# Kernel tuning notes

Measured on AMD Instinct MI355X. Metric: run time of the kernel, lower is better.

The kernel has to match this reference:

```python
import jax, jax.numpy as jnp
import numpy as np

HIDDEN = 2048
NUM_HEADS = 16
HEAD_DIM = HIDDEN // NUM_HEADS  # 128
B, S = 2, 2048


def setup_inputs() -> dict:
    key = jax.random.key(0)
    ks = jax.random.split(key, 16)
    w = lambda k, shp: (jax.random.normal(k, shp, jnp.float32) * 0.02)
    return {
        "query": jax.random.normal(ks[0], (B, S, HIDDEN), jnp.float32),
        "key": jax.random.normal(ks[1], (B, S, HIDDEN), jnp.float32),
        "value": jax.random.normal(ks[2], (B, S, HIDDEN), jnp.float32),
        "Wq": w(ks[3], (HIDDEN, HIDDEN)), "bq": jnp.zeros((HIDDEN,), jnp.float32),
        "Wk": w(ks[4], (HIDDEN, HIDDEN)), "bk": jnp.zeros((HIDDEN,), jnp.float32),
        "Wv": w(ks[5], (HIDDEN, HIDDEN)), "bv": jnp.zeros((HIDDEN,), jnp.float32),
        "Wo": w(ks[6], (HIDDEN, HIDDEN)), "bo": jnp.zeros((HIDDEN,), jnp.float32),
        "Wf1": w(ks[7], (HEAD_DIM, 2 * HEAD_DIM)), "bf1": jnp.zeros((2 * HEAD_DIM,), jnp.float32),
        "Wf2": w(ks[8], (2 * HEAD_DIM, HEAD_DIM)), "bf2": jnp.zeros((HEAD_DIM,), jnp.float32),
    }


def reference(query, key, value, Wq, bq, Wk, bk, Wv, bv, Wo, bo, Wf1, bf1, Wf2, bf2):
    b, s, _ = query.shape

    def split_heads(x):  # [b,s,H] -> [b,h,s,d]
        return x.reshape(b, s, NUM_HEADS, HEAD_DIM).transpose(0, 2, 1, 3)

    def feature_map(x):  # MLP on last dim: d -> 2d -> relu -> d
        return jax.nn.relu(x @ Wf1 + bf1) @ Wf2 + bf2

    Q = feature_map(split_heads(query @ Wq + bq))
    K = feature_map(split_heads(key @ Wk + bk))
    V = split_heads(value @ Wv + bv)

    # K^T V per head: [b,h,d,e]
    KV = jnp.einsum("bhsd,bhse->bhde", K, V)
    QKV = jnp.einsum("bhsd,bhde->bhse", Q, KV)
    # denominator: sum of all K entries per (b,h) -> scalar per head
    denom = jnp.sum(K, axis=(-2, -1), keepdims=True) + 1e-8
    QKV = QKV / denom

    context = QKV.transpose(0, 2, 1, 3).reshape(b, s, HIDDEN)
    output = context @ Wo + bo

    attn_weights = jnp.full((b, NUM_HEADS, s, s), 1.0 / s, dtype=query.dtype)
    return output, attn_weights
```

## Files before the change

kernel.cpp:

```cpp
#include <hip/hip_runtime.h>


typedef __bf16 bf16_t;
typedef __bf16 bf16x8 __attribute__((ext_vector_type(8)));
typedef __bf16 bf16x4 __attribute__((ext_vector_type(4)));
typedef float  f32x4  __attribute__((ext_vector_type(4)));

#define FILLV (1.0f / 2048.0f)

__device__ __forceinline__ void gload16(const void* g, void* l) {
  __builtin_amdgcn_global_load_lds(
      (__attribute__((address_space(1))) void*)(g),
      (__attribute__((address_space(3))) void*)(l), 16, 0, 0);
}

template<bool RELU, bool OUTF32, bool BIAS, bool FILL>
__global__ __launch_bounds__(256) void gemm_bt(
    const bf16_t* __restrict__ A, const bf16_t* __restrict__ Bt,
    const float* __restrict__ bias, void* __restrict__ C,
    int K, int lda, int ldb, int ldc,
    long aBatchB, long aBatchH, long bBatchB, long bBatchH,
    long cBatchB, long cBatchH, int HperB,
    float* __restrict__ attn, long fillBase)
{
  __shared__ bf16_t As[128 * 64];
  __shared__ bf16_t Bs[128 * 64];

  const int z  = blockIdx.z;
  const int zb = z / HperB, zh = z % HperB;
  const bf16_t* Ab = A  + (long)zb * aBatchB + (long)zh * aBatchH
                        + (long)blockIdx.y * 128 * lda;
  const bf16_t* Bb = Bt + (long)zb * bBatchB + (long)zh * bBatchH
                        + (long)blockIdx.x * 128 * ldb;

  const int t = threadIdx.x;
  const int lane = t & 63, w = t >> 6;
  const int wm = (w >> 1) * 64, wn = (w & 1) * 64;

  f32x4 acc[4][4];
#pragma unroll
  for (int i = 0; i < 4; ++i)
#pragma unroll
    for (int j = 0; j < 4; ++j) acc[i][j] = (f32x4){0.f, 0.f, 0.f, 0.f};

  for (int k0 = 0; k0 < K; k0 += 64) {
#pragma unroll
    for (int i = 0; i < 4; ++i) {
      int c = i * 256 + t;
      int row = c >> 3, col = (c & 7) * 8;
      gload16(Ab + (long)row * lda + k0 + col, &As[c * 8]);
      gload16(Bb + (long)row * ldb + k0 + col, &Bs[c * 8]);
    }
    if constexpr (FILL) {
      const f32x4 fv = {FILLV, FILLV, FILLV, FILLV};
      const int wg = blockIdx.y * gridDim.x + blockIdx.x;
      const long nB = (long)gridDim.x * gridDim.y;
      long s0 = fillBase + (((long)(k0 >> 6) * nB + wg) * 2) * 256 + t;
      __builtin_nontemporal_store(fv, (f32x4*)attn + s0);
      __builtin_nontemporal_store(fv, (f32x4*)attn + s0 + 256);
    }
    __syncthreads();
#pragma unroll
    for (int kk = 0; kk < 2; ++kk) {
      bf16x8 af[4], bfr[4];
#pragma unroll
      for (int mi = 0; mi < 4; ++mi)
        af[mi] = *(const bf16x8*)&As[(wm + mi * 16 + (lane & 15)) * 64
                                     + kk * 32 + (lane >> 4) * 8];
#pragma unroll
      for (int ni = 0; ni < 4; ++ni)
        bfr[ni] = *(const bf16x8*)&Bs[(wn + ni * 16 + (lane & 15)) * 64
                                      + kk * 32 + (lane >> 4) * 8];
#pragma unroll
      for (int mi = 0; mi < 4; ++mi)
#pragma unroll
        for (int ni = 0; ni < 4; ++ni)
          acc[mi][ni] = __builtin_amdgcn_mfma_f32_16x16x32_bf16(
              af[mi], bfr[ni], acc[mi][ni], 0, 0, 0);
    }
    __syncthreads();
  }

  const long cb = (long)zb * cBatchB + (long)zh * cBatchH;
  const int row0 = blockIdx.y * 128 + wm;
  const int col0 = blockIdx.x * 128 + wn;
#pragma unroll
  for (int mi = 0; mi < 4; ++mi) {
#pragma unroll
    for (int ni = 0; ni < 4; ++ni) {
      const int col = col0 + ni * 16 + (lane & 15);
      const float bv = BIAS ? bias[col] : 0.f;
#pragma unroll
      for (int j = 0; j < 4; ++j) {
        const int row = row0 + mi * 16 + (lane >> 4) * 4 + j;
        float v = acc[mi][ni][j] + bv;
        if (RELU) v = fmaxf(v, 0.f);
        if (OUTF32) ((float*)C)[cb + (long)row * ldc + col] = v;
        else        ((bf16_t*)C)[cb + (long)row * ldc + col] = (bf16_t)v;
      }
    }
  }
}

__global__ __launch_bounds__(256) void proj_gemm(
    const bf16_t* __restrict__ A,
    const bf16_t* __restrict__ Wt,
    const float* __restrict__ bq, const float* __restrict__ bk,
    const float* __restrict__ bv,
    bf16_t* __restrict__ C,
    float* __restrict__ attn)
{
  __shared__ bf16_t As[128 * 64];
  __shared__ bf16_t Bs[128 * 64];

  const int t = threadIdx.x;
  const int lane = t & 63, w = t >> 6;
  const int wm = (w >> 1) * 64, wn = (w & 1) * 64;
  const int which = blockIdx.y >> 5;
  const bf16_t* Ab = A + (long)blockIdx.y * 128 * 2048;
  const bf16_t* Bb = Wt + (long)which * 4194304
                        + (long)blockIdx.x * 128 * 2048;
  const float* bias = which == 0 ? bq : (which == 1 ? bk : bv);
  const int wg = blockIdx.y * 16 + blockIdx.x;
  const f32x4 fv = {FILLV, FILLV, FILLV, FILLV};

  f32x4 acc[4][4];
#pragma unroll
  for (int i = 0; i < 4; ++i)
#pragma unroll
    for (int j = 0; j < 4; ++j) acc[i][j] = (f32x4){0.f, 0.f, 0.f, 0.f};

  for (int k0 = 0; k0 < 2048; k0 += 64) {
#pragma unroll
    for (int i = 0; i < 4; ++i) {
      int c = i * 256 + t;
      int row = c >> 3, col = (c & 7) * 8;
      gload16(Ab + (long)row * 2048 + k0 + col, &As[c * 8]);
      gload16(Bb + (long)row * 2048 + k0 + col, &Bs[c * 8]);
    }
    {
      long s0 = (((long)(k0 >> 6) * 1536 + wg) * 2) * 256 + t;
      __builtin_nontemporal_store(fv, (f32x4*)attn + s0);
      __builtin_nontemporal_store(fv, (f32x4*)attn + s0 + 256);
    }
    __syncthreads();
#pragma unroll
    for (int kk = 0; kk < 2; ++kk) {
      bf16x8 af[4], bfr[4];
#pragma unroll
      for (int mi = 0; mi < 4; ++mi)
        af[mi] = *(const bf16x8*)&As[(wm + mi * 16 + (lane & 15)) * 64
                                     + kk * 32 + (lane >> 4) * 8];
#pragma unroll
      for (int ni = 0; ni < 4; ++ni)
        bfr[ni] = *(const bf16x8*)&Bs[(wn + ni * 16 + (lane & 15)) * 64
                                      + kk * 32 + (lane >> 4) * 8];
#pragma unroll
      for (int mi = 0; mi < 4; ++mi)
#pragma unroll
        for (int ni = 0; ni < 4; ++ni)
          acc[mi][ni] = __builtin_amdgcn_mfma_f32_16x16x32_bf16(
              af[mi], bfr[ni], acc[mi][ni], 0, 0, 0);
    }
    __syncthreads();
  }

  const int row0 = blockIdx.y * 128 + wm;
  const int col0 = blockIdx.x * 128 + wn;
#pragma unroll
  for (int mi = 0; mi < 4; ++mi) {
#pragma unroll
    for (int ni = 0; ni < 4; ++ni) {
      const int col = col0 + ni * 16 + (lane & 15);
      const float bvv = bias[col];
#pragma unroll
      for (int j = 0; j < 4; ++j) {
        const int row = row0 + mi * 16 + (lane >> 4) * 4 + j;
        C[(long)row * 2048 + col] = (bf16_t)(acc[mi][ni][j] + bvv);
      }
    }
  }
}

__global__ __launch_bounds__(256) void fm_fused(
    const bf16_t* __restrict__ A, const bf16_t* __restrict__ W1t,
    const bf16_t* __restrict__ W2t, const float* __restrict__ b1,
    const float* __restrict__ b2, bf16_t* __restrict__ Out)
{
  __shared__ char Hs[64 * 256 * 2];
  const int t = threadIdx.x, lane = t & 63, w = t >> 6;
  const long r0 = (long)blockIdx.x * 64;
  const int lr = lane & 15, lk = lane >> 4;

  f32x4 acc[4][4];
#pragma unroll
  for (int i = 0; i < 4; ++i)
#pragma unroll
    for (int j = 0; j < 4; ++j) acc[i][j] = (f32x4){0.f, 0.f, 0.f, 0.f};
  const int wn = w * 64;
#pragma unroll
  for (int kk = 0; kk < 4; ++kk) {
    bf16x8 af[4], bfr[4];
#pragma unroll
    for (int mi = 0; mi < 4; ++mi)
      af[mi] = *(const bf16x8*)&A[(r0 + mi * 16 + lr) * 128 + kk * 32 + lk * 8];
#pragma unroll
    for (int ni = 0; ni < 4; ++ni)
      bfr[ni] = *(const bf16x8*)&W1t[(long)(wn + ni * 16 + lr) * 128
                                     + kk * 32 + lk * 8];
#pragma unroll
    for (int mi = 0; mi < 4; ++mi)
#pragma unroll
      for (int ni = 0; ni < 4; ++ni)
        acc[mi][ni] = __builtin_amdgcn_mfma_f32_16x16x32_bf16(
            af[mi], bfr[ni], acc[mi][ni], 0, 0, 0);
  }
#pragma unroll
  for (int ni = 0; ni < 4; ++ni) {
    const int col = wn + ni * 16 + lr;
    const float bvv = b1[col];
#pragma unroll
    for (int mi = 0; mi < 4; ++mi)
#pragma unroll
      for (int j = 0; j < 4; ++j) {
        const int row = mi * 16 + lk * 4 + j;
        float h = fmaxf(acc[mi][ni][j] + bvv, 0.f);
        int byte = (row << 9) + (col << 1);
        byte ^= (row & 7) << 4;
        *(bf16_t*)(Hs + byte) = (bf16_t)h;
      }
  }
  __syncthreads();

  f32x4 acc2[4][2];
#pragma unroll
  for (int i = 0; i < 4; ++i)
#pragma unroll
    for (int j = 0; j < 2; ++j) acc2[i][j] = (f32x4){0.f, 0.f, 0.f, 0.f};
  const int wn2 = w * 32;
#pragma unroll
  for (int kk = 0; kk < 8; ++kk) {
    bf16x8 af[4], bfr[2];
#pragma unroll
    for (int mi = 0; mi < 4; ++mi) {
      const int m = mi * 16 + lr;
      int byte = (m << 9) + kk * 64 + lk * 16;
      byte ^= (m & 7) << 4;
      af[mi] = *(const bf16x8*)(Hs + byte);
    }
#pragma unroll
    for (int ni = 0; ni < 2; ++ni)
      bfr[ni] = *(const bf16x8*)&W2t[(long)(wn2 + ni * 16 + lr) * 256
                                     + kk * 32 + lk * 8];
#pragma unroll
    for (int mi = 0; mi < 4; ++mi)
#pragma unroll
      for (int ni = 0; ni < 2; ++ni)
        acc2[mi][ni] = __builtin_amdgcn_mfma_f32_16x16x32_bf16(
            af[mi], bfr[ni], acc2[mi][ni], 0, 0, 0);
  }
#pragma unroll
  for (int ni = 0; ni < 2; ++ni) {
    const int col = wn2 + ni * 16 + lr;
    const float bvv = b2[col];
#pragma unroll
    for (int mi = 0; mi < 4; ++mi)
#pragma unroll
      for (int j = 0; j < 4; ++j) {
        const int row = mi * 16 + lk * 4 + j;
        Out[(r0 + row) * 128 + col] = (bf16_t)(acc2[mi][ni][j] + bvv);
      }
  }
}

__global__ __launch_bounds__(256) void prep(
    const float* __restrict__ q, const float* __restrict__ k,
    const float* __restrict__ v,
    const float* __restrict__ Wq, const float* __restrict__ Wk,
    const float* __restrict__ Wv, const float* __restrict__ Wo,
    const float* __restrict__ Wf1, const float* __restrict__ Wf2,
    bf16_t* __restrict__ qkv_bf, bf16_t* __restrict__ Wqkv_t,
    bf16_t* __restrict__ Wf1_t, bf16_t* __restrict__ Wf2_t)
{
  const int t = threadIdx.x;
  const int bid = blockIdx.x;
  __shared__ float tile[32][33];

  if (bid < 24576) {
    const float* in = bid < 8192 ? q : (bid < 16384 ? k : v);
    bf16_t* o = qkv_bf + (long)(bid >> 13) * 8388608L;
    long i = ((long)(bid & 8191) * 256 + t) * 4;
    float4 x = *(const float4*)&in[i];
    bf16x4 r = {(bf16_t)x.x, (bf16_t)x.y, (bf16_t)x.z, (bf16_t)x.w};
    *(bf16x4*)&o[i] = r;
    return;
  }

  const int x = t & 31, y = t >> 5;
  const float* W; bf16_t* out; int Kd, Nd, n0, k0;
  if (bid < 40960) {
    const int sub = bid - 24576;
    const int z = sub >> 12, r = sub & 4095;
    W = z == 0 ? Wq : z == 1 ? Wk : z == 2 ? Wv : Wo;
    out = Wqkv_t + (long)z * 4194304L;
    Kd = 2048; Nd = 2048;
    n0 = (r & 63) * 32; k0 = (r >> 6) * 32;
  } else if (bid < 40992) {
    const int sub = bid - 40960;
    W = Wf1; out = Wf1_t; Kd = 128; Nd = 256;
    n0 = (sub & 7) * 32; k0 = (sub >> 3) * 32;
  } else {
    const int sub = bid - 40992;
    W = Wf2; out = Wf2_t; Kd = 256; Nd = 128;
    n0 = (sub & 3) * 32; k0 = (sub >> 2) * 32;
  }
#pragma unroll
  for (int j = 0; j < 32; j += 8)
    tile[y + j][x] = W[(long)(k0 + y + j) * Nd + n0 + x];
  __syncthreads();
#pragma unroll
  for (int j = 0; j < 32; j += 8)
    out[(long)(n0 + y + j) * Kd + k0 + x] = (bf16_t)tile[x][y + j];
}

__global__ __launch_bounds__(256) void kv_partial(
    const bf16_t* __restrict__ Kf, const bf16_t* __restrict__ Vp,
    float* __restrict__ part, float* __restrict__ part_denom) {
  const int z = blockIdx.y, b = z >> 4, h = z & 15;
  const int s0 = blockIdx.x * 128;
  const int t = threadIdx.x;
  __shared__ bf16_t Ks[32 * 128];
  __shared__ bf16_t Vs[32 * 128];
  __shared__ float red[4];
  const bf16_t* Kb = Kf + (long)b * 4194304 + h * 128;
  const bf16_t* Vb = Vp + (long)b * 4194304 + h * 128;
  float acc[8][8];
#pragma unroll
  for (int i = 0; i < 8; ++i)
#pragma unroll
    for (int j = 0; j < 8; ++j) acc[i][j] = 0.f;
  float ksum = 0.f;
  const int d0 = (t & 15) * 8, e0 = (t >> 4) * 8;
  for (int sc = 0; sc < 128; sc += 32) {
#pragma unroll
    for (int i = 0; i < 2; ++i) {
      int idx = (i * 256 + t) * 8;
      int r = idx >> 7, c = idx & 127;
      long g = (long)(s0 + sc + r) * 2048 + c;
      *(bf16x8*)&Ks[r * 128 + c] = *(const bf16x8*)&Kb[g];
      *(bf16x8*)&Vs[r * 128 + c] = *(const bf16x8*)&Vb[g];
    }
    __syncthreads();
    {
      bf16x8 a0 = *(const bf16x8*)&Ks[t * 16];
      bf16x8 a1 = *(const bf16x8*)&Ks[t * 16 + 8];
#pragma unroll
      for (int j = 0; j < 8; ++j) ksum += (float)a0[j] + (float)a1[j];
    }
    for (int s = 0; s < 32; ++s) {
      bf16x8 kv = *(const bf16x8*)&Ks[s * 128 + d0];
      bf16x8 vv = *(const bf16x8*)&Vs[s * 128 + e0];
      float kf[8], vf[8];
#pragma unroll
      for (int i = 0; i < 8; ++i) { kf[i] = (float)kv[i]; vf[i] = (float)vv[i]; }
#pragma unroll
      for (int i = 0; i < 8; ++i)
#pragma unroll
        for (int j = 0; j < 8; ++j) acc[i][j] += vf[i] * kf[j];
    }
    __syncthreads();
  }

#pragma unroll
  for (int off = 32; off; off >>= 1) ksum += __shfl_down(ksum, off, 64);
  if ((t & 63) == 0) red[t >> 6] = ksum;
  __syncthreads();
  if (t == 0)
    part_denom[blockIdx.x * 32 + z] = red[0] + red[1] + red[2] + red[3];

  float* pb = part + ((long)blockIdx.x * 32 + z) * 16384;
#pragma unroll
  for (int i = 0; i < 8; ++i)
#pragma unroll
    for (int j = 0; j < 8; ++j)
      pb[(e0 + i) * 128 + (d0 + j)] = acc[i][j];
}

__global__ __launch_bounds__(256) void kv_reduce(
    const float* __restrict__ part, const float* __restrict__ part_denom,
    bf16_t* __restrict__ KVT) {
  const int z = blockIdx.x >> 4, slice = blockIdx.x & 15;
  const int t = threadIdx.x;
  float dsum = 0.f;
#pragma unroll
  for (int c = 0; c < 16; ++c) dsum += part_denom[c * 32 + z];
  const float inv = 1.0f / (dsum + 1e-8f);
  const int base = slice * 1024;
  for (int i = base + t; i < base + 1024; i += 256) {
    float s = 0.f;
#pragma unroll
    for (int c = 0; c < 16; ++c) s += part[((long)c * 32 + z) * 16384 + i];
    KVT[(long)z * 16384 + i] = (bf16_t)(s * inv);
  }
}

extern "C" void kernel_launch(void* const* d_in, const int* in_sizes, int n_in,
                              void* d_out, int out_size, void* d_ws, size_t ws_size,
                              hipStream_t stream) {
  (void)in_sizes; (void)n_in; (void)out_size; (void)ws_size;
  const float* q   = (const float*)d_in[0];
  const float* k   = (const float*)d_in[1];
  const float* v   = (const float*)d_in[2];
  const float* Wq  = (const float*)d_in[3];
  const float* bq  = (const float*)d_in[4];
  const float* Wk  = (const float*)d_in[5];
  const float* bk  = (const float*)d_in[6];
  const float* Wv  = (const float*)d_in[7];
  const float* bv  = (const float*)d_in[8];
  const float* Wo  = (const float*)d_in[9];
  const float* bo  = (const float*)d_in[10];
  const float* Wf1 = (const float*)d_in[11];
  const float* bf1 = (const float*)d_in[12];
  const float* Wf2 = (const float*)d_in[13];
  const float* bf2 = (const float*)d_in[14];

  bf16_t* P      = (bf16_t*)d_ws;
  bf16_t* qkv_bf = P;
  bf16_t* Wqkv_t = P + 25165824L;
  bf16_t* Wo_t   = P + 37748736L;
  bf16_t* Wf1_t  = P + 41943040L;
  bf16_t* Wf2_t  = P + 41975808L;
  bf16_t* Qp     = P + 42008576L;
  bf16_t* Vp     = P + 58785792L;
  bf16_t* Qf     = P + 83951616L;
  bf16_t* Kf     = P + 92340224L;
  bf16_t* KVT    = P + 100728832L;
  float*  part   = (float*)d_ws;
  float*  part_denom = (float*)d_ws + 8388608L;

  float* out0 = (float*)d_out;
  float* attn = (float*)d_out + 8388608L;

  dim3 blk(256);

  prep<<<41024, blk, 0, stream>>>(q, k, v, Wq, Wk, Wv, Wo, Wf1, Wf2,
                                  qkv_bf, Wqkv_t, Wf1_t, Wf2_t);

  proj_gemm<<<dim3(16, 96), blk, 0, stream>>>(
      qkv_bf, Wqkv_t, bq, bk, bv, Qp, attn);

  fm_fused<<<2048, blk, 0, stream>>>(Qp, Wf1_t, Wf2_t, bf1, bf2, Qf);

  kv_partial<<<dim3(16, 32), blk, 0, stream>>>(Kf, Vp, part, part_denom);

  kv_reduce<<<512, blk, 0, stream>>>(part, part_denom, KVT);

  gemm_bt<false, false, false, false><<<dim3(1, 16, 32), blk, 0, stream>>>(
      Qf, KVT, nullptr, Vp, 128, 2048, 128, 2048,
      4194304L, 128L, 262144L, 16384L, 4194304L, 128L, 16,
      nullptr, 0);

  gemm_bt<false, true, true, true><<<dim3(16, 32, 1), blk, 0, stream>>>(
      Vp, Wo_t, bo, out0, 2048, 2048, 2048, 2048, 0, 0, 0, 0, 0, 0, 1,
      attn, 25165824L);
}
```

Before: 363.8 us.

## Use 256x256 double-buffered QKV GEMM and spread attn fill across kernels

Replaces the 128x128 QKV projection GEMM with a 512-thread, 256x256-tile kernel. It double-buffers LDS with XOR-swizzled layout, splits global loads into quarter stages interleaved with MFMA phases, and raises the MFMA phases' wave priority. The constant attn_weights fill is redistributed: each of the smaller kernels (fm_fused, kv_partial, kv_reduce, the batched QKV GEMM) writes a slice in its epilogue, and the output GEMM writes three slots per k-step instead of two. The aim is better MFMA utilization and data reuse in the dominant GEMM, with the bandwidth-bound fill hidden under compute-light kernels. The risks are the large LDS footprint limiting occupancy and mistakes in the fill offset bookkeeping.

```diff
diff --git a/kernel.cpp b/kernel.cpp
--- a/kernel.cpp
+++ b/kernel.cpp
@@ -8,20 +8,204 @@
 
 #define FILLV (1.0f / 2048.0f)
 
+#define VMCNT2() asm volatile("s_waitcnt vmcnt(2)" ::: "memory")
+#define VMCNT0() asm volatile("s_waitcnt vmcnt(0)" ::: "memory")
+#define LGKM0()  asm volatile("s_waitcnt lgkmcnt(0)" ::: "memory")
+#define BAR()    __builtin_amdgcn_s_barrier()
+#define SCHED0() __builtin_amdgcn_sched_barrier(0)
+
 __device__ __forceinline__ void gload16(const void* g, void* l) {
   __builtin_amdgcn_global_load_lds(
       (__attribute__((address_space(1))) void*)(g),
       (__attribute__((address_space(3))) void*)(l), 16, 0, 0);
 }
 
-template<bool RELU, bool OUTF32, bool BIAS, bool FILL>
+__device__ __forceinline__ void fill_epilogue(float* attn, long slotBase,
+                                              int slots, int t) {
+  const f32x4 fv = {FILLV, FILLV, FILLV, FILLV};
+  f32x4* dst = (f32x4*)attn + slotBase + t;
+  for (int i = 0; i < slots; i += 256)
+    __builtin_nontemporal_store(fv, dst + i);
+}
+
+__device__ __forceinline__ void stage_half(const bf16_t* __restrict__ g,
+                                           int h, unsigned char* ldsT, int t) {
+  const bf16_t* gh = g + (long)h * 128 * 2048;
+  unsigned char* lh = ldsT + h * 16384;
+#pragma unroll
+  for (int i = 0; i < 2; ++i) {
+    const int c = t + i * 512;
+    const int r = c >> 3;
+    const int cc = ((c & 7) ^ (r & 7)) * 8;
+    gload16(gh + (long)r * 2048 + cc, lh + c * 16);
+  }
+}
+
+__device__ __forceinline__ bf16x8 lds_frag(const unsigned char* base,
+                                           int row, int kelem) {
+  int byte = row * 128 + kelem * 2;
+  byte ^= (row & 7) << 4;
+  return *(const bf16x8*)(base + byte);
+}
+
+__global__ __launch_bounds__(512, 2) void proj_gemm8(
+    const bf16_t* __restrict__ A, const bf16_t* __restrict__ Wt,
+    const float* __restrict__ bq, const float* __restrict__ bk,
+    const float* __restrict__ bv, bf16_t* __restrict__ C,
+    float* __restrict__ attn)
+{
+  __shared__ __align__(16) unsigned char smem[131072];
+  const int t = threadIdx.x;
+  const int lane = t & 63;
+  const int wid = t >> 6;
+  const int wr = wid >> 2, wc = wid & 3;
+  const int bid = blockIdx.x;
+  const int bx = bid & 7, by = bid >> 3;
+  const int which = by >> 4;
+  const bf16_t* Ab = A + (long)by * 256 * 2048;
+  const bf16_t* Bb = Wt + (long)which * 4194304 + (long)bx * 256 * 2048;
+  const float* bias = which == 0 ? bq : (which == 1 ? bk : bv);
+
+  const int lr = lane & 15;
+  const int l8 = (lane >> 4) * 8;
+
+  f32x4 acc[8][4];
+#pragma unroll
+  for (int i = 0; i < 8; ++i)
+#pragma unroll
+    for (int j = 0; j < 4; ++j) acc[i][j] = (f32x4){0.f, 0.f, 0.f, 0.f};
+
+  stage_half(Ab, 0, smem, t);
+  stage_half(Ab, 1, smem, t);
+  stage_half(Bb, 0, smem + 32768, t);
+  stage_half(Bb, 1, smem + 32768, t);
+
+  bf16x8 aF[4][2], bF[4][2];
+
+  for (int kt = 0; kt < 32; ++kt) {
+    const int cur = kt & 1;
+    unsigned char* curA = smem + cur * 65536;
+    unsigned char* curB = curA + 32768;
+    unsigned char* nxtA = smem + (cur ^ 1) * 65536;
+    unsigned char* nxtB = nxtA + 32768;
+    const bool hn = kt < 31;
+    const bf16_t* An = Ab + (kt + 1) * 64;
+    const bf16_t* Bn = Bb + (kt + 1) * 64;
+    const int arow = wr * 128 + lr;
+    const int brow = wc * 64 + lr;
+
+    if (hn) { stage_half(An, 0, nxtA, t); VMCNT2(); }
+    else    { VMCNT0(); }
+    BAR();
+#pragma unroll
+    for (int mi = 0; mi < 4; ++mi)
+#pragma unroll
+      for (int kk = 0; kk < 2; ++kk)
+        aF[mi][kk] = lds_frag(curA, arow + mi * 16, kk * 32 + l8);
+#pragma unroll
+    for (int ni = 0; ni < 2; ++ni)
+#pragma unroll
+      for (int kk = 0; kk < 2; ++kk)
+        bF[ni][kk] = lds_frag(curB, brow + ni * 16, kk * 32 + l8);
+    LGKM0(); SCHED0();
+    __builtin_amdgcn_s_setprio(1);
+#pragma unroll
+    for (int mi = 0; mi < 4; ++mi)
+#pragma unroll
+      for (int ni = 0; ni < 2; ++ni)
+#pragma unroll
+        for (int kk = 0; kk < 2; ++kk)
+          acc[mi][ni] = __builtin_amdgcn_mfma_f32_16x16x32_bf16(
+              aF[mi][kk], bF[ni][kk], acc[mi][ni], 0, 0, 0);
+    __builtin_amdgcn_s_setprio(0);
+    BAR();
+
+    if (hn) stage_half(An, 1, nxtA, t);
+#pragma unroll
+    for (int ni = 0; ni < 2; ++ni)
+#pragma unroll
+      for (int kk = 0; kk < 2; ++kk)
+        bF[2 + ni][kk] = lds_frag(curB, brow + (2 + ni) * 16, kk * 32 + l8);
+    BAR(); LGKM0(); SCHED0();
+    __builtin_amdgcn_s_setprio(1);
+#pragma unroll
+    for (int mi = 0; mi < 4; ++mi)
+#pragma unroll
+      for (int ni = 0; ni < 2; ++ni)
+#pragma unroll
+        for (int kk = 0; kk < 2; ++kk)
+          acc[mi][2 + ni] = __builtin_amdgcn_mfma_f32_16x16x32_bf16(
+              aF[mi][kk], bF[2 + ni][kk], acc[mi][2 + ni], 0, 0, 0);
+    __builtin_amdgcn_s_setprio(0);
+    BAR();
+
+    if (hn) stage_half(Bn, 0, nxtB, t);
+#pragma unroll
+    for (int mi = 0; mi < 4; ++mi)
+#pragma unroll
+      for (int kk = 0; kk < 2; ++kk)
+        aF[mi][kk] = lds_frag(curA, arow + 64 + mi * 16, kk * 32 + l8);
+    BAR(); LGKM0(); SCHED0();
+    __builtin_amdgcn_s_setprio(1);
+#pragma unroll
+    for (int mi = 0; mi < 4; ++mi)
+#pragma unroll
+      for (int ni = 0; ni < 2; ++ni)
+#pragma unroll
+        for (int kk = 0; kk < 2; ++kk)
+          acc[4 + mi][ni] = __builtin_amdgcn_mfma_f32_16x16x32_bf16(
+              aF[mi][kk], bF[ni][kk], acc[4 + mi][ni], 0, 0, 0);
+    __builtin_amdgcn_s_setprio(0);
+    BAR();
+
+    if (hn) stage_half(Bn, 1, nxtB, t);
+    BAR(); LGKM0(); SCHED0();
+    __builtin_amdgcn_s_setprio(1);
+#pragma unroll
+    for (int mi = 0; mi < 4; ++mi)
+#pragma unroll
+      for (int ni = 0; ni < 2; ++ni)
+#pragma unroll
+        for (int kk = 0; kk < 2; ++kk)
+          acc[4 + mi][2 + ni] = __builtin_amdgcn_mfma_f32_16x16x32_bf16(
+              aF[mi][kk], bF[2 + ni][kk], acc[4 + mi][2 + ni], 0, 0, 0);
+    __builtin_amdgcn_s_setprio(0);
+    BAR();
+  }
+
+  {
+    const f32x4 fv = {FILLV, FILLV, FILLV, FILLV};
+    f32x4* dst = (f32x4*)attn + 27262976L + (long)bid * 16384 + t;
+#pragma unroll
+    for (int i = 0; i < 16384; i += 512)
+      __builtin_nontemporal_store(fv, dst + i);
+  }
+
+  const int row0 = by * 256 + wr * 128;
+  const int col0 = bx * 256 + wc * 64;
+#pragma unroll
+  for (int mi = 0; mi < 8; ++mi) {
+#pragma unroll
+    for (int ni = 0; ni < 4; ++ni) {
+      const int col = col0 + ni * 16 + lr;
+      const float bvv = bias[col];
+#pragma unroll
+      for (int j = 0; j < 4; ++j) {
+        const int row = row0 + mi * 16 + (lane >> 4) * 4 + j;
+        C[(long)row * 2048 + col] = (bf16_t)(acc[mi][ni][j] + bvv);
+      }
+    }
+  }
+}
+
+template<bool RELU, bool OUTF32, bool BIAS, int FILLMODE>
 __global__ __launch_bounds__(256) void gemm_bt(
     const bf16_t* __restrict__ A, const bf16_t* __restrict__ Bt,
     const float* __restrict__ bias, void* __restrict__ C,
     int K, int lda, int ldb, int ldc,
     long aBatchB, long aBatchH, long bBatchB, long bBatchH,
     long cBatchB, long cBatchH, int HperB,
-    float* __restrict__ attn, long fillBase)
+    float* __restrict__ attn, long fillBase, int fillSlots)
 {
   __shared__ bf16_t As[128 * 64];
   __shared__ bf16_t Bs[128 * 64];
@@ -36,6 +220,8 @@
   const int t = threadIdx.x;
   const int lane = t & 63, w = t >> 6;
   const int wm = (w >> 1) * 64, wn = (w & 1) * 64;
+  const int p = ((int)blockIdx.z * gridDim.y + blockIdx.y) * gridDim.x
+                + blockIdx.x;
 
   f32x4 acc[4][4];
 #pragma unroll
@@ -51,13 +237,13 @@
       gload16(Ab + (long)row * lda + k0 + col, &As[c * 8]);
       gload16(Bb + (long)row * ldb + k0 + col, &Bs[c * 8]);
     }
-    if constexpr (FILL) {
+    if constexpr (FILLMODE == 1) {
       const f32x4 fv = {FILLV, FILLV, FILLV, FILLV};
-      const int wg = blockIdx.y * gridDim.x + blockIdx.x;
-      const long nB = (long)gridDim.x * gridDim.y;
-      long s0 = fillBase + (((long)(k0 >> 6) * nB + wg) * 2) * 256 + t;
+      const long nB = (long)gridDim.x * gridDim.y * gridDim.z;
+      long s0 = fillBase + (((long)(k0 >> 6) * nB + p) * 3) * 256 + t;
       __builtin_nontemporal_store(fv, (f32x4*)attn + s0);
       __builtin_nontemporal_store(fv, (f32x4*)attn + s0 + 256);
+      __builtin_nontemporal_store(fv, (f32x4*)attn + s0 + 512);
     }
     __syncthreads();
 #pragma unroll
@@ -80,6 +266,9 @@
     }
     __syncthreads();
   }
+
+  if constexpr (FILLMODE == 2)
+    fill_epilogue(attn, fillBase + (long)p * fillSlots, fillSlots, t);
 
   const long cb = (long)zb * cBatchB + (long)zh * cBatchH;
   const int row0 = blockIdx.y * 128 + wm;
@@ -102,90 +291,11 @@
   }
 }
 
-__global__ __launch_bounds__(256) void proj_gemm(
-    const bf16_t* __restrict__ A,
-    const bf16_t* __restrict__ Wt,
-    const float* __restrict__ bq, const float* __restrict__ bk,
-    const float* __restrict__ bv,
-    bf16_t* __restrict__ C,
-    float* __restrict__ attn)
-{
-  __shared__ bf16_t As[128 * 64];
-  __shared__ bf16_t Bs[128 * 64];
-
-  const int t = threadIdx.x;
-  const int lane = t & 63, w = t >> 6;
-  const int wm = (w >> 1) * 64, wn = (w & 1) * 64;
-  const int which = blockIdx.y >> 5;
-  const bf16_t* Ab = A + (long)blockIdx.y * 128 * 2048;
-  const bf16_t* Bb = Wt + (long)which * 4194304
-                        + (long)blockIdx.x * 128 * 2048;
-  const float* bias = which == 0 ? bq : (which == 1 ? bk : bv);
-  const int wg = blockIdx.y * 16 + blockIdx.x;
-  const f32x4 fv = {FILLV, FILLV, FILLV, FILLV};
-
-  f32x4 acc[4][4];
-#pragma unroll
-  for (int i = 0; i < 4; ++i)
-#pragma unroll
-    for (int j = 0; j < 4; ++j) acc[i][j] = (f32x4){0.f, 0.f, 0.f, 0.f};
-
-  for (int k0 = 0; k0 < 2048; k0 += 64) {
-#pragma unroll
-    for (int i = 0; i < 4; ++i) {
-      int c = i * 256 + t;
-      int row = c >> 3, col = (c & 7) * 8;
-      gload16(Ab + (long)row * 2048 + k0 + col, &As[c * 8]);
-      gload16(Bb + (long)row * 2048 + k0 + col, &Bs[c * 8]);
-    }
-    {
-      long s0 = (((long)(k0 >> 6) * 1536 + wg) * 2) * 256 + t;
-      __builtin_nontemporal_store(fv, (f32x4*)attn + s0);
-      __builtin_nontemporal_store(fv, (f32x4*)attn + s0 + 256);
-    }
-    __syncthreads();
-#pragma unroll
-    for (int kk = 0; kk < 2; ++kk) {
-      bf16x8 af[4], bfr[4];
-#pragma unroll
-      for (int mi = 0; mi < 4; ++mi)
-        af[mi] = *(const bf16x8*)&As[(wm + mi * 16 + (lane & 15)) * 64
-                                     + kk * 32 + (lane >> 4) * 8];
-#pragma unroll
-      for (int ni = 0; ni < 4; ++ni)
-        bfr[ni] = *(const bf16x8*)&Bs[(wn + ni * 16 + (lane & 15)) * 64
-                                      + kk * 32 + (lane >> 4) * 8];
-#pragma unroll
-      for (int mi = 0; mi < 4; ++mi)
-#pragma unroll
-        for (int ni = 0; ni < 4; ++ni)
-          acc[mi][ni] = __builtin_amdgcn_mfma_f32_16x16x32_bf16(
-              af[mi], bfr[ni], acc[mi][ni], 0, 0, 0);
-    }
-    __syncthreads();
-  }
-
-  const int row0 = blockIdx.y * 128 + wm;
-  const int col0 = blockIdx.x * 128 + wn;
-#pragma unroll
-  for (int mi = 0; mi < 4; ++mi) {
-#pragma unroll
-    for (int ni = 0; ni < 4; ++ni) {
-      const int col = col0 + ni * 16 + (lane & 15);
-      const float bvv = bias[col];
-#pragma unroll
-      for (int j = 0; j < 4; ++j) {
-        const int row = row0 + mi * 16 + (lane >> 4) * 4 + j;
-        C[(long)row * 2048 + col] = (bf16_t)(acc[mi][ni][j] + bvv);
-      }
-    }
-  }
-}
-
 __global__ __launch_bounds__(256) void fm_fused(
     const bf16_t* __restrict__ A, const bf16_t* __restrict__ W1t,
     const bf16_t* __restrict__ W2t, const float* __restrict__ b1,
-    const float* __restrict__ b2, bf16_t* __restrict__ Out)
+    const float* __restrict__ b2, bf16_t* __restrict__ Out,
+    float* __restrict__ attn)
 {
   __shared__ char Hs[64 * 256 * 2];
   const int t = threadIdx.x, lane = t & 63, w = t >> 6;
@@ -259,6 +369,9 @@
         acc2[mi][ni] = __builtin_amdgcn_mfma_f32_16x16x32_bf16(
             af[mi], bfr[ni], acc2[mi][ni], 0, 0, 0);
   }
+
+  fill_epilogue(attn, 12582912L + (long)blockIdx.x * 2048, 2048, t);
+
 #pragma unroll
   for (int ni = 0; ni < 2; ++ni) {
     const int col = wn2 + ni * 16 + lr;
@@ -325,7 +438,8 @@
 
 __global__ __launch_bounds__(256) void kv_partial(
     const bf16_t* __restrict__ Kf, const bf16_t* __restrict__ Vp,
-    float* __restrict__ part, float* __restrict__ part_denom) {
+    float* __restrict__ part, float* __restrict__ part_denom,
+    float* __restrict__ attn) {
   const int z = blockIdx.y, b = z >> 4, h = z & 15;
   const int s0 = blockIdx.x * 128;
   const int t = threadIdx.x;
@@ -378,6 +492,9 @@
   if (t == 0)
     part_denom[blockIdx.x * 32 + z] = red[0] + red[1] + red[2] + red[3];
 
+  fill_epilogue(attn,
+      16777216L + (long)(blockIdx.y * 16 + blockIdx.x) * 8192, 8192, t);
+
   float* pb = part + ((long)blockIdx.x * 32 + z) * 16384;
 #pragma unroll
   for (int i = 0; i < 8; ++i)
@@ -388,7 +505,7 @@
 
 __global__ __launch_bounds__(256) void kv_reduce(
     const float* __restrict__ part, const float* __restrict__ part_denom,
-    bf16_t* __restrict__ KVT) {
+    bf16_t* __restrict__ KVT, float* __restrict__ attn) {
   const int z = blockIdx.x >> 4, slice = blockIdx.x & 15;
   const int t = threadIdx.x;
   float dsum = 0.f;
@@ -402,6 +519,7 @@
     for (int c = 0; c < 16; ++c) s += part[((long)c * 32 + z) * 16384 + i];
     KVT[(long)z * 16384 + i] = (bf16_t)(s * inv);
   }
+  fill_epilogue(attn, 20971520L + (long)blockIdx.x * 4096, 4096, t);
 }
 
 extern "C" void kernel_launch(void* const* d_in, const int* in_sizes, int n_in,
@@ -446,21 +564,20 @@
   prep<<<41024, blk, 0, stream>>>(q, k, v, Wq, Wk, Wv, Wo, Wf1, Wf2,
                                   qkv_bf, Wqkv_t, Wf1_t, Wf2_t);
 
-  proj_gemm<<<dim3(16, 96), blk, 0, stream>>>(
-      qkv_bf, Wqkv_t, bq, bk, bv, Qp, attn);
-
-  fm_fused<<<2048, blk, 0, stream>>>(Qp, Wf1_t, Wf2_t, bf1, bf2, Qf);
-
-  kv_partial<<<dim3(16, 32), blk, 0, stream>>>(Kf, Vp, part, part_denom);
-
-  kv_reduce<<<512, blk, 0, stream>>>(part, part_denom, KVT);
-
-  gemm_bt<false, false, false, false><<<dim3(1, 16, 32), blk, 0, stream>>>(
+  proj_gemm8<<<384, 512, 0, stream>>>(qkv_bf, Wqkv_t, bq, bk, bv, Qp, attn);
+
+  fm_fused<<<2048, blk, 0, stream>>>(Qp, Wf1_t, Wf2_t, bf1, bf2, Qf, attn);
+
+  kv_partial<<<dim3(16, 32), blk, 0, stream>>>(Kf, Vp, part, part_denom, attn);
+
+  kv_reduce<<<512, blk, 0, stream>>>(part, part_denom, KVT, attn);
+
+  gemm_bt<false, false, false, 2><<<dim3(1, 16, 32), blk, 0, stream>>>(
       Qf, KVT, nullptr, Vp, 128, 2048, 128, 2048,
       4194304L, 128L, 262144L, 16384L, 4194304L, 128L, 16,
-      nullptr, 0);
-
-  gemm_bt<false, true, true, true><<<dim3(16, 32, 1), blk, 0, stream>>>(
+      attn, 23068672L, 8192);
+
+  gemm_bt<false, true, true, 1><<<dim3(16, 32, 1), blk, 0, stream>>>(
       Vp, Wo_t, bo, out0, 2048, 2048, 2048, 2048, 0, 0, 0, 0, 0, 0, 1,
-      attn, 25165824L);
-}
+      attn, 0L, 0);
+}
```

Result: no change. 359.5 us (-1.2%).
